# Kernel tuning notes

Measured on AMD Instinct MI355X. Metric: run time of the kernel, lower is better.

## Reference

```python
import jax, jax.numpy as jnp
import numpy as np

GROUPS = 8
EPS = 1e-5


def group_norm(x, gamma, beta):
    # x: [B,H,W,C]; normalize per group over (H, W, C/g)
    B, H, W, C = x.shape
    g = GROUPS
    xg = x.reshape(B, H, W, g, C // g)
    mean = jnp.mean(xg, axis=(1, 2, 4), keepdims=True)
    var = jnp.var(xg, axis=(1, 2, 4), keepdims=True)
    xg = (xg - mean) / jnp.sqrt(var + EPS)
    return gamma * xg.reshape(B, H, W, C) + beta


def setup_inputs() -> dict:
    key = jax.random.key(0)
    ks = jax.random.split(key, 6)
    B, H, W, C = 8, 64, 64, 128
    s = 1.0 / np.sqrt(C)
    return {
        "x": jax.random.normal(ks[0], (B, H, W, C), jnp.float32),
        "gamma": jnp.ones((C,), jnp.float32),
        "beta": jnp.zeros((C,), jnp.float32),
        "wq": jax.random.normal(ks[1], (C, C), jnp.float32) * s,
        "bq": jnp.zeros((C,), jnp.float32),
        "wk": jax.random.normal(ks[2], (C, C), jnp.float32) * s,
        "bk": jnp.zeros((C,), jnp.float32),
        "wv": jax.random.normal(ks[3], (C, C), jnp.float32) * s,
        "bv": jnp.zeros((C,), jnp.float32),
        "wp": jax.random.normal(ks[4], (C, C), jnp.float32) * s,
        "bp": jnp.zeros((C,), jnp.float32),
    }


def reference(x, gamma, beta, wq, bq, wk, bk, wv, bv, wp, bp):
    B, H, W, C = x.shape
    scale = jnp.asarray(C, jnp.float32) ** -0.5
    xn = group_norm(x, gamma, beta)  # note: residual uses normalized input (as in source)
    N = H * W
    xf = xn.reshape(B, N, C)
    q = xf @ wq + bq
    k = xf @ wk + bk
    v = xf @ wv + bv
    attn = jnp.einsum('bnc,bmc->bnm', q, k) * scale  # [B, N, N]
    attn = jax.nn.softmax(attn, axis=-1)
    out = jnp.einsum('bnm,bmc->bnc', attn, v)
    out = out @ wp + bp
    return (xf + out).reshape(B, H, W, C)
```

## Files before the change

### kernel.cpp

```cpp
#include <hip/hip_runtime.h>
#include <hip/hip_bf16.h>

#define B_ 8
#define N_ 4096
#define C_ 128
#define EPSV 1e-5f
#define SPLIT 2
#define KVB 64

using bf8   = __attribute__((ext_vector_type(8))) short;
using u16x8 = __attribute__((ext_vector_type(8))) ushort;
using f32x4 = __attribute__((ext_vector_type(4))) float;

__device__ __forceinline__ ushort f2b(float f) {
  __hip_bfloat16 h = __float2bfloat16(f);
  return *reinterpret_cast<ushort*>(&h);
}
__device__ __forceinline__ float b2f(ushort u) {
  union { float f; unsigned x; } t; t.x = ((unsigned)u) << 16; return t.f;
}

__device__ __forceinline__ void gll16(const void* g, void* l) {
  __builtin_amdgcn_global_load_lds((const __attribute__((address_space(1))) void*)g,
                                   (__attribute__((address_space(3))) void*)l,
                                   16, 0, 0);
}

__global__ __launch_bounds__(256) void gnw(const float* __restrict__ x,
                                           const float* __restrict__ wq,
                                           const float* __restrict__ wk,
                                           const float* __restrict__ wv,
                                           const float* __restrict__ wp,
                                           float2* __restrict__ part,
                                           ushort* __restrict__ wt) {
  if (blockIdx.y >= 64) {
    const int widx = blockIdx.y - 64;
    const float* w = (widx == 0) ? wq : (widx == 1) ? wk : (widx == 2) ? wv : wp;
    ushort* o = wt + widx * 16384;
    const int r  = blockIdx.x * 16 + (threadIdx.x >> 4);
    const int c0 = (threadIdx.x & 15) << 3;
    const float4 v0 = *reinterpret_cast<const float4*>(w + (size_t)r * C_ + c0);
    const float4 v1 = *reinterpret_cast<const float4*>(w + (size_t)r * C_ + c0 + 4);
    const float vv[8] = {v0.x, v0.y, v0.z, v0.w, v1.x, v1.y, v1.z, v1.w};
    #pragma unroll
    for (int j = 0; j < 8; ++j) {
      const int n = c0 + j;
      const int el = (r & 7) | ((((r >> 3)) ^ (n & 7)) << 3);
      o[(size_t)n * C_ + el] = f2b(vv[j]);
    }
    return;
  }
  const int bg = blockIdx.y;
  const int b = bg >> 3, g = bg & 7;
  const int chunk = blockIdx.x;
  const float* xp = x + (size_t)b * N_ * C_ + g * 16;
  float s = 0.f, s2 = 0.f;
  const int base4 = chunk * 2048;
  for (int i = threadIdx.x; i < 2048; i += 256) {
    const int idx = base4 + i;
    const int n = idx >> 2, c4 = (idx & 3) << 2;
    const float4 v = *reinterpret_cast<const float4*>(xp + (size_t)n * C_ + c4);
    s  += v.x + v.y + v.z + v.w;
    s2 += v.x*v.x + v.y*v.y + v.z*v.z + v.w*v.w;
  }
  #pragma unroll
  for (int off = 32; off; off >>= 1) { s += __shfl_down(s, off); s2 += __shfl_down(s2, off); }
  __shared__ float red[8];
  const int wid = threadIdx.x >> 6;
  if ((threadIdx.x & 63) == 0) { red[wid] = s; red[4 + wid] = s2; }
  __syncthreads();
  if (threadIdx.x == 0)
    part[bg * 8 + chunk] = make_float2(red[0]+red[1]+red[2]+red[3],
                                       red[4]+red[5]+red[6]+red[7]);
}

__device__ __forceinline__ void block_mrs(const float2* part, int b, int tid,
                                          float2* sp, float* mrs) {
  if (tid < 64) sp[tid] = part[b * 64 + tid];
  __syncthreads();
  if (tid < 8) {
    float s = 0.f, s2 = 0.f;
    #pragma unroll
    for (int c = 0; c < 8; ++c) { s += sp[tid*8+c].x; s2 += sp[tid*8+c].y; }
    const float inv = 1.f / 65536.f;
    const float m = s * inv;
    const float var = s2 * inv - m * m;
    mrs[tid*2]   = m;
    mrs[tid*2+1] = rsqrtf(var + EPSV);
  }
  __syncthreads();
}

__global__ __launch_bounds__(256) void qkv_fused(const float* __restrict__ x,
                                                 const float2* __restrict__ part,
                                                 const float* __restrict__ gamma,
                                                 const float* __restrict__ beta,
                                                 const ushort* __restrict__ wt,
                                                 const float* __restrict__ bq,
                                                 const float* __restrict__ bk,
                                                 const float* __restrict__ bv,
                                                 ushort* __restrict__ qb, ushort* __restrict__ kb,
                                                 ushort* __restrict__ vtb) {
  __shared__ ushort A[64][128];
  __shared__ ushort Bt[128][128];
  __shared__ float2 sp[64];
  __shared__ float mrs[16];
  const int m0 = blockIdx.x * 64;
  const int tid = threadIdx.x;
  const int wid = tid >> 6, lane = tid & 63;
  block_mrs(part, m0 >> 12, tid, sp, mrs);
  for (int i = tid; i < 1024; i += 256) {
    const int row = i >> 4, c = (i & 15) << 3;
    const int grow = m0 + row;
    const float mm = mrs[(c >> 4) * 2], rr = mrs[(c >> 4) * 2 + 1];
    const float4 v0 = *reinterpret_cast<const float4*>(&x[(size_t)grow * C_ + c]);
    const float4 v1 = *reinterpret_cast<const float4*>(&x[(size_t)grow * C_ + c + 4]);
    const float vv[8] = {v0.x, v0.y, v0.z, v0.w, v1.x, v1.y, v1.z, v1.w};
    u16x8 u;
    #pragma unroll
    for (int j = 0; j < 8; ++j)
      u[j] = f2b((vv[j] - mm) * rr * gamma[c+j] + beta[c+j]);
    const int el = ((c >> 3) ^ (row & 7)) << 3;
    *reinterpret_cast<u16x8*>(&A[row][el]) = u;
  }
  const int wm = wid >> 1, wn = wid & 1;
  const int lr = lane & 15, lk = lane >> 4;
  const float qscale = 0.12751749f;

  #pragma unroll 1
  for (int j = 0; j < 3; ++j) {
    const ushort* wtj = wt + j * 16384;
    const float* bias = (j == 0) ? bq : (j == 1) ? bk : bv;
    __syncthreads();
    {
      ushort* bt0 = &Bt[0][0];
      #pragma unroll
      for (int c8 = 0; c8 < 8; ++c8) {
        const int ch = wid * 8 + c8;
        gll16(wtj + ch * 512 + lane * 8, bt0 + ch * 512);
      }
    }
    __syncthreads();
    f32x4 acc[2][4] = {};
    #pragma unroll
    for (int ks = 0; ks < 4; ++ks) {
      const int g0 = ks * 4 + lk;
      bf8 af[2], bfv[4];
      #pragma unroll
      for (int mi = 0; mi < 2; ++mi) {
        const int row = wm * 32 + mi * 16 + lr;
        af[mi] = *reinterpret_cast<const bf8*>(&A[row][(g0 ^ (row & 7)) << 3]);
      }
      #pragma unroll
      for (int ni = 0; ni < 4; ++ni) {
        const int n = wn * 64 + ni * 16 + lr;
        bfv[ni] = *reinterpret_cast<const bf8*>(&Bt[n][(g0 ^ (n & 7)) << 3]);
      }
      #pragma unroll
      for (int mi = 0; mi < 2; ++mi)
        #pragma unroll
        for (int ni = 0; ni < 4; ++ni)
          acc[mi][ni] = __builtin_amdgcn_mfma_f32_16x16x32_bf16(af[mi], bfv[ni], acc[mi][ni], 0, 0, 0);
    }
    if (j < 2) {
      ushort* out = (j == 0) ? qb : kb;
      const float sc = (j == 0) ? qscale : 1.0f;
      #pragma unroll
      for (int mi = 0; mi < 2; ++mi)
        #pragma unroll
        for (int ni = 0; ni < 4; ++ni)
          #pragma unroll
          for (int r = 0; r < 4; ++r) {
            const int row = m0 + wm * 32 + mi * 16 + lk * 4 + r;
            const int col = wn * 64 + ni * 16 + lr;
            out[(size_t)row * C_ + col] = f2b((acc[mi][ni][r] + bias[col]) * sc);
          }
    } else {
      #pragma unroll
      for (int mi = 0; mi < 2; ++mi)
        #pragma unroll
        for (int ni = 0; ni < 4; ++ni) {
          const int rowb = m0 + wm * 32 + mi * 16 + lk * 4;
          const int col  = wn * 64 + ni * 16 + lr;
          const int bb = rowb >> 12, nn = rowb & 4095;
          const int o  = nn & 63;
          const int op = (o & 0x23) | ((o & 0x0C) << 1) | ((o & 0x10) >> 2);
          const int nnp = (nn & ~63) | op;
          const float bv2 = bias[col];
          ushort4 u;
          u.x = f2b(acc[mi][ni][0] + bv2);
          u.y = f2b(acc[mi][ni][1] + bv2);
          u.z = f2b(acc[mi][ni][2] + bv2);
          u.w = f2b(acc[mi][ni][3] + bv2);
          *reinterpret_cast<ushort4*>(&vtb[((size_t)bb * C_ + col) * N_ + nnp]) = u;
        }
    }
  }
}

__global__ __launch_bounds__(256, 2) void attn_fwd(const ushort* __restrict__ q,
                                                   const ushort* __restrict__ k,
                                                   const ushort* __restrict__ vt,
                                                   ushort* __restrict__ Op,
                                                   float* __restrict__ lsum) {
  extern __shared__ ushort smem[];
  const int bid = blockIdx.x;
  const int b   = bid & 7;
  const int qi  = (bid >> 3) & 31;
  const int z   = bid >> 8;
  const int q0  = qi * 128;
  const int tid = threadIdx.x;
  const int w = tid >> 6, lane = tid & 63;
  const int lr = lane & 15, lk = lane >> 4;
  const ushort* qb = q  + (size_t)b * N_ * C_;
  const ushort* kb = k  + (size_t)b * N_ * C_;
  const ushort* vb = vt + (size_t)b * C_ * N_;

  bf8 qf[2][4];
  #pragma unroll
  for (int h = 0; h < 2; ++h) {
    const int qrow = q0 + w * 32 + h * 16 + lr;
    #pragma unroll
    for (int ks = 0; ks < 4; ++ks)
      qf[h][ks] = *reinterpret_cast<const bf8*>(&qb[(size_t)qrow * C_ + ks * 32 + lk * 8]);
  }

  bf8 onesf;
  #pragma unroll
  for (int j = 0; j < 8; ++j) onesf[j] = (short)0x3F80;

  f32x4 oacc[2][8] = {};
  f32x4 accl[2] = {};

  const int krow_in = lane >> 4;
  const int kslot   = lane & 15;
  const int vrow_in = lane >> 3;
  const int vslot   = lane & 7;

  const int t0 = z * (64 / SPLIT);
  const int t1 = (z + 1) * (64 / SPLIT);

  auto STAGE = [&](int sel, int kt) {
    const int kv0 = kt * KVB;
    ushort* Kd = smem + sel * 8192;
    ushort* Vd = smem + 16384 + sel * 8192;
    #pragma unroll
    for (int j = 0; j < 4; ++j) {
      const int m = w * 4 + j;
      const int krow = m * 4 + krow_in;
      gll16(kb + (size_t)(kv0 + krow) * C_ + ((kslot ^ (krow & 7)) << 3),
            Kd + m * 512);
      const int vrow = m * 8 + vrow_in;
      gll16(vb + (size_t)vrow * N_ + kv0 + ((vslot ^ (vrow & 7)) << 3),
            Vd + m * 512);
    }
  };

  STAGE(0, t0);
  for (int kt = t0; kt < t1; ++kt) {
    const int cur = (kt - t0) & 1;
    __syncthreads();
    if (kt + 1 < t1) STAGE(cur ^ 1, kt + 1);

    const ushort* Kc = smem + cur * 8192;
    const ushort* Vc = smem + 16384 + cur * 8192;

    f32x4 s[2][4] = {};
    __builtin_amdgcn_s_setprio(1);
    #pragma unroll
    for (int ks = 0; ks < 4; ++ks) {
      const int g0 = ks * 4 + lk;
      bf8 kf[4];
      #pragma unroll
      for (int ni = 0; ni < 4; ++ni) {
        const int n = ni * 16 + lr;
        kf[ni] = *reinterpret_cast<const bf8*>(&Kc[n * 128 + ((g0 ^ (n & 7)) << 3)]);
      }
      #pragma unroll
      for (int h = 0; h < 2; ++h)
        #pragma unroll
        for (int ni = 0; ni < 4; ++ni)
          s[h][ni] = __builtin_amdgcn_mfma_f32_16x16x32_bf16(kf[ni], qf[h][ks], s[h][ni], 0, 0, 0);
    }
    __builtin_amdgcn_s_setprio(0);

    bf8 pa[2][2];
    #pragma unroll
    for (int kss = 0; kss < 2; ++kss)
      #pragma unroll
      for (int h = 0; h < 2; ++h) {
        bf8 t;
        #pragma unroll
        for (int hi = 0; hi < 2; ++hi) {
          const f32x4 sv = s[h][kss * 2 + hi];
          #pragma unroll
          for (int r = 0; r < 4; ++r)
            t[hi * 4 + r] = (short)f2b(__builtin_amdgcn_exp2f(sv[r]));
        }
        pa[kss][h] = t;
      }

    __builtin_amdgcn_s_setprio(1);
    #pragma unroll
    for (int kss = 0; kss < 2; ++kss) {
      #pragma unroll
      for (int h = 0; h < 2; ++h)
        accl[h] = __builtin_amdgcn_mfma_f32_16x16x32_bf16(pa[kss][h], onesf, accl[h], 0, 0, 0);
      const int g = kss * 4 + lk;
      #pragma unroll
      for (int ni = 0; ni < 8; ++ni) {
        const int d = ni * 16 + lr;
        const bf8 vf = *reinterpret_cast<const bf8*>(&Vc[d * 64 + ((g ^ (d & 7)) << 3)]);
        #pragma unroll
        for (int h = 0; h < 2; ++h)
          oacc[h][ni] = __builtin_amdgcn_mfma_f32_16x16x32_bf16(pa[kss][h], vf, oacc[h][ni], 0, 0, 0);
      }
    }
    __builtin_amdgcn_s_setprio(0);
  }

  const size_t zb = (size_t)(z * B_ + b);
  if (lr == 0) {
    #pragma unroll
    for (int h = 0; h < 2; ++h)
      #pragma unroll
      for (int r = 0; r < 4; ++r)
        lsum[zb * N_ + q0 + w * 32 + h * 16 + lk * 4 + r] = accl[h][r];
  }
  ushort* ob = Op + zb * N_ * C_;
  #pragma unroll
  for (int h = 0; h < 2; ++h)
    #pragma unroll
    for (int ni = 0; ni < 8; ++ni)
      #pragma unroll
      for (int r = 0; r < 4; ++r) {
        const int row = q0 + w * 32 + h * 16 + lk * 4 + r;
        ob[(size_t)row * C_ + ni * 16 + lr] = f2b(oacc[h][ni][r]);
      }
}

__global__ __launch_bounds__(256) void proj_res(const ushort* __restrict__ Op,
                                                const float* __restrict__ lsum,
                                                const ushort* __restrict__ wtp,
                                                const float* __restrict__ bias,
                                                const float* __restrict__ x,
                                                const float2* __restrict__ part,
                                                const float* __restrict__ gamma,
                                                const float* __restrict__ beta,
                                                float* __restrict__ outp) {
  __shared__ ushort A[64][128];
  __shared__ ushort Bt[128][128];
  __shared__ float2 sp[64];
  __shared__ float mrs[16];
  const int m0 = blockIdx.x * 64;
  const int tid = threadIdx.x;
  const int wid = tid >> 6, lane = tid & 63;
  const size_t BN = (size_t)B_ * N_;
  block_mrs(part, m0 >> 12, tid, sp, mrs);
  {
    ushort* bt0 = &Bt[0][0];
    #pragma unroll
    for (int c8 = 0; c8 < 8; ++c8) {
      const int ch = wid * 8 + c8;
      gll16(wtp + ch * 512 + lane * 8, bt0 + ch * 512);
    }
  }
  for (int i = tid; i < 1024; i += 256) {
    const int row = i >> 4, c = (i & 15) << 3;
    const size_t grow = m0 + row;
    float l = 0.f;
    #pragma unroll
    for (int zz = 0; zz < SPLIT; ++zz) l += lsum[zz * BN + grow];
    const float inv = 1.f / l;
    float acc8[8] = {};
    #pragma unroll
    for (int zz = 0; zz < SPLIT; ++zz) {
      const u16x8 a = *reinterpret_cast<const u16x8*>(&Op[(zz * BN + grow) * C_ + c]);
      #pragma unroll
      for (int j = 0; j < 8; ++j) acc8[j] += b2f(a[j]);
    }
    u16x8 u;
    #pragma unroll
    for (int j = 0; j < 8; ++j) u[j] = f2b(acc8[j] * inv);
    const int el = ((c >> 3) ^ (row & 7)) << 3;
    *reinterpret_cast<u16x8*>(&A[row][el]) = u;
  }
  __syncthreads();
  const int wm = wid >> 1, wn = wid & 1;
  const int lr = lane & 15, lk = lane >> 4;
  f32x4 acc[2][4] = {};
  #pragma unroll
  for (int ks = 0; ks < 4; ++ks) {
    const int g0 = ks * 4 + lk;
    bf8 af[2], bfv[4];
    #pragma unroll
    for (int mi = 0; mi < 2; ++mi) {
      const int row = wm * 32 + mi * 16 + lr;
      af[mi] = *reinterpret_cast<const bf8*>(&A[row][(g0 ^ (row & 7)) << 3]);
    }
    #pragma unroll
    for (int ni = 0; ni < 4; ++ni) {
      const int n = wn * 64 + ni * 16 + lr;
      bfv[ni] = *reinterpret_cast<const bf8*>(&Bt[n][(g0 ^ (n & 7)) << 3]);
    }
    #pragma unroll
    for (int mi = 0; mi < 2; ++mi)
      #pragma unroll
      for (int ni = 0; ni < 4; ++ni)
        acc[mi][ni] = __builtin_amdgcn_mfma_f32_16x16x32_bf16(af[mi], bfv[ni], acc[mi][ni], 0, 0, 0);
  }
  #pragma unroll
  for (int mi = 0; mi < 2; ++mi)
    #pragma unroll
    for (int ni = 0; ni < 4; ++ni) {
      const int col = wn * 64 + ni * 16 + lr;
      const float gmm = gamma[col], bta = beta[col], bia = bias[col];
      const float mm = mrs[(col >> 4) * 2], rr = mrs[(col >> 4) * 2 + 1];
      #pragma unroll
      for (int r = 0; r < 4; ++r) {
        const int row = m0 + wm * 32 + mi * 16 + lk * 4 + r;
        const float xn = (x[(size_t)row * C_ + col] - mm) * rr * gmm + bta;
        outp[(size_t)row * C_ + col] = xn + acc[mi][ni][r] + bia;
      }
    }
}

extern "C" void kernel_launch(void* const* d_in, const int* in_sizes, int n_in,
                              void* d_out, int out_size, void* d_ws, size_t ws_size,
                              hipStream_t stream) {
  const float* x     = (const float*)d_in[0];
  const float* gamma = (const float*)d_in[1];
  const float* beta  = (const float*)d_in[2];
  const float* wq    = (const float*)d_in[3];
  const float* bq    = (const float*)d_in[4];
  const float* wk    = (const float*)d_in[5];
  const float* bk    = (const float*)d_in[6];
  const float* wv    = (const float*)d_in[7];
  const float* bv    = (const float*)d_in[8];
  const float* wp    = (const float*)d_in[9];
  const float* bp    = (const float*)d_in[10];
  float* outp = (float*)d_out;

  char* ws = (char*)d_ws;
  const size_t MB8 = (size_t)B_ * N_ * C_ * 2;
  float2* part = (float2*)(ws + 512);
  ushort* qb   = (ushort*)(ws + 8192);
  ushort* kb   = (ushort*)(ws + 8192 + MB8);
  ushort* vtb  = (ushort*)(ws + 8192 + 2*MB8);
  ushort* Op   = (ushort*)(ws + 8192 + 3*MB8);
  float*  lsum = (float*)(ws + 8192 + (3 + SPLIT)*MB8);
  ushort* wt   = (ushort*)(ws + 8192 + (3 + SPLIT)*MB8 + (size_t)SPLIT*B_*N_*4);

  gnw<<<dim3(8, 68), 256, 0, stream>>>(x, wq, wk, wv, wp, part, wt);
  qkv_fused<<<512, 256, 0, stream>>>(x, part, gamma, beta, wt,
                                     bq, bk, bv, qb, kb, vtb);
  (void)hipFuncSetAttribute((const void*)attn_fwd,
                            hipFuncAttributeMaxDynamicSharedMemorySize, 65536);
  attn_fwd<<<dim3(32 * B_ * SPLIT), 256, 65536, stream>>>(qb, kb, vtb, Op, lsum);
  proj_res<<<512, 256, 0, stream>>>(Op, lsum, wt + 3 * 16384, bp, x, part, gamma, beta, outp);
}
```

Before: 97.10 us.

## Shrink attention tiles to 64 queries and 32-key blocks for higher occupancy

The attention kernel now gives each wave 16 query rows instead of 32 and stages 32-key KV blocks instead of 64. It halves LDS per block, doubles the grid and raises launch bounds to four blocks per CU. The V-transpose layout and swizzle in the QKV epilogue are rewritten to match the new 32-wide block. The aim is to cut register and LDS pressure and hide latency through occupancy, at the cost of less K/V reuse per LDS load and twice as many barrier iterations.

New measurement: 115.8 us. +19.3%, slower.

```diff
diff --git a/kernel.cpp b/kernel.cpp
--- a/kernel.cpp
+++ b/kernel.cpp
@@ -6,7 +6,7 @@
 #define C_ 128
 #define EPSV 1e-5f
 #define SPLIT 2
-#define KVB 64
+#define KVB 32
 
 using bf8   = __attribute__((ext_vector_type(8))) short;
 using u16x8 = __attribute__((ext_vector_type(8))) ushort;
@@ -183,9 +183,9 @@
           const int rowb = m0 + wm * 32 + mi * 16 + lk * 4;
           const int col  = wn * 64 + ni * 16 + lr;
           const int bb = rowb >> 12, nn = rowb & 4095;
-          const int o  = nn & 63;
-          const int op = (o & 0x23) | ((o & 0x0C) << 1) | ((o & 0x10) >> 2);
-          const int nnp = (nn & ~63) | op;
+          const int o  = nn & 31;
+          const int op = (o & 3) | ((o & 0x0C) << 1) | ((o & 0x10) >> 2);
+          const int nnp = (nn & ~31) | op;
           const float bv2 = bias[col];
           ushort4 u;
           u.x = f2b(acc[mi][ni][0] + bv2);
@@ -198,7 +198,7 @@
   }
 }
 
-__global__ __launch_bounds__(256, 2) void attn_fwd(const ushort* __restrict__ q,
+__global__ __launch_bounds__(256, 4) void attn_fwd(const ushort* __restrict__ q,
                                                    const ushort* __restrict__ k,
                                                    const ushort* __restrict__ vt,
                                                    ushort* __restrict__ Op,
@@ -206,137 +206,111 @@
   extern __shared__ ushort smem[];
   const int bid = blockIdx.x;
   const int b   = bid & 7;
-  const int qi  = (bid >> 3) & 31;
-  const int z   = bid >> 8;
-  const int q0  = qi * 128;
+  const int qi  = (bid >> 3) & 63;
+  const int z   = bid >> 9;
   const int tid = threadIdx.x;
   const int w = tid >> 6, lane = tid & 63;
   const int lr = lane & 15, lk = lane >> 4;
+  const int q0 = qi * 64 + w * 16;
   const ushort* qb = q  + (size_t)b * N_ * C_;
   const ushort* kb = k  + (size_t)b * N_ * C_;
   const ushort* vb = vt + (size_t)b * C_ * N_;
 
-  bf8 qf[2][4];
-  #pragma unroll
-  for (int h = 0; h < 2; ++h) {
-    const int qrow = q0 + w * 32 + h * 16 + lr;
-    #pragma unroll
-    for (int ks = 0; ks < 4; ++ks)
-      qf[h][ks] = *reinterpret_cast<const bf8*>(&qb[(size_t)qrow * C_ + ks * 32 + lk * 8]);
-  }
+  bf8 qf[4];
+  #pragma unroll
+  for (int ks = 0; ks < 4; ++ks)
+    qf[ks] = *reinterpret_cast<const bf8*>(&qb[(size_t)(q0 + lr) * C_ + ks * 32 + lk * 8]);
 
   bf8 onesf;
   #pragma unroll
   for (int j = 0; j < 8; ++j) onesf[j] = (short)0x3F80;
 
-  f32x4 oacc[2][8] = {};
-  f32x4 accl[2] = {};
-
-  const int krow_in = lane >> 4;
-  const int kslot   = lane & 15;
-  const int vrow_in = lane >> 3;
-  const int vslot   = lane & 7;
-
-  const int t0 = z * (64 / SPLIT);
-  const int t1 = (z + 1) * (64 / SPLIT);
-
-  auto STAGE = [&](int sel, int kt) {
+  f32x4 oacc[8] = {};
+  f32x4 accl = {};
+
+  const int t0 = z * 64;
+  const int t1 = t0 + 64;
+
+  auto STAGE_K = [&](int sel, int kt) {
     const int kv0 = kt * KVB;
-    ushort* Kd = smem + sel * 8192;
-    ushort* Vd = smem + 16384 + sel * 8192;
-    #pragma unroll
-    for (int j = 0; j < 4; ++j) {
-      const int m = w * 4 + j;
-      const int krow = m * 4 + krow_in;
-      gll16(kb + (size_t)(kv0 + krow) * C_ + ((kslot ^ (krow & 7)) << 3),
+    ushort* Kd = smem + sel * 4096;
+    #pragma unroll
+    for (int j = 0; j < 2; ++j) {
+      const int m = w * 2 + j;
+      const int krow = m * 4 + (lane >> 4);
+      gll16(kb + (size_t)(kv0 + krow) * C_ + (((lane & 15) ^ (krow & 7)) << 3),
             Kd + m * 512);
-      const int vrow = m * 8 + vrow_in;
-      gll16(vb + (size_t)vrow * N_ + kv0 + ((vslot ^ (vrow & 7)) << 3),
-            Vd + m * 512);
     }
   };
-
-  STAGE(0, t0);
+  auto STAGE_V = [&](int sel, int kt) {
+    const int kv0 = kt * KVB;
+    ushort* Vd = smem + 8192 + sel * 4096;
+    #pragma unroll
+    for (int j = 0; j < 2; ++j) {
+      const int m = w * 2 + j;
+      const int dd = m * 8 + (lane >> 3);
+      const int sl = lane & 7;
+      const int d  = dd * 2 + (sl >> 2);
+      const int g  = (sl & 3) ^ (dd & 3);
+      gll16(vb + (size_t)d * N_ + kv0 + g * 8, Vd + m * 512);
+    }
+  };
+
+  STAGE_K(0, t0);
+  STAGE_V(0, t0);
+  __builtin_amdgcn_s_setprio(1);
+  #pragma unroll 1
   for (int kt = t0; kt < t1; ++kt) {
     const int cur = (kt - t0) & 1;
     __syncthreads();
-    if (kt + 1 < t1) STAGE(cur ^ 1, kt + 1);
-
-    const ushort* Kc = smem + cur * 8192;
-    const ushort* Vc = smem + 16384 + cur * 8192;
-
-    f32x4 s[2][4] = {};
-    __builtin_amdgcn_s_setprio(1);
+    if (kt + 1 < t1) { STAGE_K(cur ^ 1, kt + 1); STAGE_V(cur ^ 1, kt + 1); }
+
+    const ushort* Kc = smem + cur * 4096;
+    const ushort* Vc = smem + 8192 + cur * 4096;
+
+    f32x4 s0 = {}, s1 = {};
     #pragma unroll
     for (int ks = 0; ks < 4; ++ks) {
       const int g0 = ks * 4 + lk;
-      bf8 kf[4];
-      #pragma unroll
-      for (int ni = 0; ni < 4; ++ni) {
-        const int n = ni * 16 + lr;
-        kf[ni] = *reinterpret_cast<const bf8*>(&Kc[n * 128 + ((g0 ^ (n & 7)) << 3)]);
-      }
-      #pragma unroll
-      for (int h = 0; h < 2; ++h)
-        #pragma unroll
-        for (int ni = 0; ni < 4; ++ni)
-          s[h][ni] = __builtin_amdgcn_mfma_f32_16x16x32_bf16(kf[ni], qf[h][ks], s[h][ni], 0, 0, 0);
-    }
-    __builtin_amdgcn_s_setprio(0);
-
-    bf8 pa[2][2];
-    #pragma unroll
-    for (int kss = 0; kss < 2; ++kss)
-      #pragma unroll
-      for (int h = 0; h < 2; ++h) {
-        bf8 t;
-        #pragma unroll
-        for (int hi = 0; hi < 2; ++hi) {
-          const f32x4 sv = s[h][kss * 2 + hi];
-          #pragma unroll
-          for (int r = 0; r < 4; ++r)
-            t[hi * 4 + r] = (short)f2b(__builtin_amdgcn_exp2f(sv[r]));
-        }
-        pa[kss][h] = t;
-      }
-
-    __builtin_amdgcn_s_setprio(1);
-    #pragma unroll
-    for (int kss = 0; kss < 2; ++kss) {
-      #pragma unroll
-      for (int h = 0; h < 2; ++h)
-        accl[h] = __builtin_amdgcn_mfma_f32_16x16x32_bf16(pa[kss][h], onesf, accl[h], 0, 0, 0);
-      const int g = kss * 4 + lk;
-      #pragma unroll
-      for (int ni = 0; ni < 8; ++ni) {
-        const int d = ni * 16 + lr;
-        const bf8 vf = *reinterpret_cast<const bf8*>(&Vc[d * 64 + ((g ^ (d & 7)) << 3)]);
-        #pragma unroll
-        for (int h = 0; h < 2; ++h)
-          oacc[h][ni] = __builtin_amdgcn_mfma_f32_16x16x32_bf16(pa[kss][h], vf, oacc[h][ni], 0, 0, 0);
-      }
-    }
-    __builtin_amdgcn_s_setprio(0);
-  }
+      const int sw = (g0 ^ (lr & 7)) << 3;
+      const bf8 kf0 = *reinterpret_cast<const bf8*>(&Kc[lr * 128 + sw]);
+      const bf8 kf1 = *reinterpret_cast<const bf8*>(&Kc[(16 + lr) * 128 + sw]);
+      s0 = __builtin_amdgcn_mfma_f32_16x16x32_bf16(kf0, qf[ks], s0, 0, 0, 0);
+      s1 = __builtin_amdgcn_mfma_f32_16x16x32_bf16(kf1, qf[ks], s1, 0, 0, 0);
+    }
+
+    bf8 pa;
+    #pragma unroll
+    for (int r = 0; r < 4; ++r) {
+      pa[r]     = (short)f2b(__builtin_amdgcn_exp2f(s0[r]));
+      pa[4 + r] = (short)f2b(__builtin_amdgcn_exp2f(s1[r]));
+    }
+    accl = __builtin_amdgcn_mfma_f32_16x16x32_bf16(pa, onesf, accl, 0, 0, 0);
+
+    #pragma unroll
+    for (int ni = 0; ni < 8; ++ni) {
+      const int d = ni * 16 + lr;
+      const int off = (d >> 1) * 64 + ((((d & 1) << 2) | (lk ^ ((d >> 1) & 3))) << 3);
+      const bf8 vf = *reinterpret_cast<const bf8*>(&Vc[off]);
+      oacc[ni] = __builtin_amdgcn_mfma_f32_16x16x32_bf16(pa, vf, oacc[ni], 0, 0, 0);
+    }
+  }
+  __builtin_amdgcn_s_setprio(0);
 
   const size_t zb = (size_t)(z * B_ + b);
   if (lr == 0) {
     #pragma unroll
-    for (int h = 0; h < 2; ++h)
-      #pragma unroll
-      for (int r = 0; r < 4; ++r)
-        lsum[zb * N_ + q0 + w * 32 + h * 16 + lk * 4 + r] = accl[h][r];
+    for (int r = 0; r < 4; ++r)
+      lsum[zb * N_ + q0 + lk * 4 + r] = accl[r];
   }
   ushort* ob = Op + zb * N_ * C_;
   #pragma unroll
-  for (int h = 0; h < 2; ++h)
-    #pragma unroll
-    for (int ni = 0; ni < 8; ++ni)
-      #pragma unroll
-      for (int r = 0; r < 4; ++r) {
-        const int row = q0 + w * 32 + h * 16 + lk * 4 + r;
-        ob[(size_t)row * C_ + ni * 16 + lr] = f2b(oacc[h][ni][r]);
-      }
+  for (int ni = 0; ni < 8; ++ni)
+    #pragma unroll
+    for (int r = 0; r < 4; ++r) {
+      const int row = q0 + lk * 4 + r;
+      ob[(size_t)row * C_ + ni * 16 + lr] = f2b(oacc[ni][r]);
+    }
 }
 
 __global__ __launch_bounds__(256) void proj_res(const ushort* __restrict__ Op,
@@ -455,7 +429,7 @@
   qkv_fused<<<512, 256, 0, stream>>>(x, part, gamma, beta, wt,
                                      bq, bk, bv, qb, kb, vtb);
   (void)hipFuncSetAttribute((const void*)attn_fwd,
-                            hipFuncAttributeMaxDynamicSharedMemorySize, 65536);
-  attn_fwd<<<dim3(32 * B_ * SPLIT), 256, 65536, stream>>>(qb, kb, vtb, Op, lsum);
+                            hipFuncAttributeMaxDynamicSharedMemorySize, 32768);
+  attn_fwd<<<dim3(64 * B_ * SPLIT), 256, 32768, stream>>>(qb, kb, vtb, Op, lsum);
   proj_res<<<512, 256, 0, stream>>>(Op, lsum, wt + 3 * 16384, bp, x, part, gamma, beta, outp);
 }
```
